# Kernel optimization log

Hardware: AMD Instinct MI355X
Metric: run time of the kernel (lower is better)

## Reference

```python
import jax, jax.numpy as jnp
import numpy as np

C = 128          # feature channels
N = 1_048_576    # octree nodes at depth 6 (divisible by 8)
M = 262_144      # full parent node count at depth 5 (incl. empty nodes)


def setup_inputs() -> dict:
    key = jax.random.key(0)
    k1, k2, k3 = jax.random.split(key, 3)
    data = jax.random.normal(k1, (C, N), dtype=jnp.float32)
    idx = jax.random.randint(k2, (M,), 0, N // 8, dtype=jnp.int32)
    empty = jax.random.uniform(k3, (M,)) < 0.5
    child_idx = jnp.where(empty, jnp.int32(-1), idx)  # -1 => empty (zero pad)
    return {"data": data, "child_idx": child_idx}


def reference(data, child_idx):
    # octree_max_pool: every 8 consecutive sibling nodes -> 1 parent value
    c, n = data.shape
    grouped = data.reshape(c, n // 8, 8)          # [C, N/8, 8]
    pooled = grouped.max(axis=-1)                  # [C, N/8]
    # octree_pad: scatter pooled non-empty parents into full parent node list,
    # zero-filling empty nodes (child_idx == -1).
    safe = jnp.clip(child_idx, 0, None)            # safe gather index
    out = jnp.where(child_idx[None, :] >= 0, pooled[:, safe], jnp.float32(0))
    return out                                     # [C, M]
```

## Files before the change

kernel.cpp:

```cpp
#include <hip/hip_runtime.h>


#define CH 128
#define CH_PER_BLOCK 8

__global__ __launch_bounds__(256) void octree_maxpool_kernel(
    const float* __restrict__ data,
    const int* __restrict__ child_idx,
    float* __restrict__ out,
    int n,
    int m_total)
{
    int m = blockIdx.x * 256 + threadIdx.x;
    if (m >= m_total) return;

    int idx = child_idx[m];
    int c0 = blockIdx.y * CH_PER_BLOCK;

    if (idx < 0) {
        #pragma unroll
        for (int cc = 0; cc < CH_PER_BLOCK; ++cc) {
            out[(size_t)(c0 + cc) * m_total + m] = 0.0f;
        }
        return;
    }

    size_t base = (size_t)idx * 8;
    #pragma unroll
    for (int cc = 0; cc < CH_PER_BLOCK; ++cc) {
        const float4* p = (const float4*)(data + (size_t)(c0 + cc) * n + base);
        float4 a = p[0];
        float4 b = p[1];
        float v = fmaxf(fmaxf(fmaxf(a.x, a.y), fmaxf(a.z, a.w)),
                        fmaxf(fmaxf(b.x, b.y), fmaxf(b.z, b.w)));
        out[(size_t)(c0 + cc) * m_total + m] = v;
    }
}

extern "C" void kernel_launch(void* const* d_in, const int* in_sizes, int n_in,
                              void* d_out, int out_size, void* d_ws, size_t ws_size,
                              hipStream_t stream) {
    const float* data      = (const float*)d_in[0];
    const int*   child_idx = (const int*)d_in[1];
    float*       out       = (float*)d_out;

    int n = in_sizes[0] / CH;
    int m = in_sizes[1];

    dim3 block(256, 1, 1);
    dim3 grid((m + 255) / 256, CH / CH_PER_BLOCK, 1);
    hipLaunchKernelGGL(octree_maxpool_kernel, grid, block, 0, stream,
                       data, child_idx, out, n, m);
}
```

Measured before the change: 864.8 us.

## Split into streaming pool pass and small gather-pad pass via workspace

The fused kernel is replaced by two kernels whenever the workspace is large enough. The first streams the whole input contiguously and writes an 8x smaller pooled buffer. The second gathers single floats from that pooled buffer, which is compact enough to stay largely in cache, and zero-fills the empty parents. This swaps random 32-byte gathers from the large input for one coalesced pass plus gathers from a small buffer, at the cost of reading data that empty nodes never use and an extra kernel launch. The fused path remains as a fallback when the workspace is too small.

New measurement: 833.6 us. 3.6% less time.

```diff
diff --git a/kernel.cpp b/kernel.cpp
--- a/kernel.cpp
+++ b/kernel.cpp
@@ -4,36 +4,69 @@
 #define CH 128
 #define CH_PER_BLOCK 8
 
-__global__ __launch_bounds__(256) void octree_maxpool_kernel(
+__global__ __launch_bounds__(256) void pool_kernel(
     const float* __restrict__ data,
+    float* __restrict__ pooled,
+    int total_groups)
+{
+    int g = blockIdx.x * 256 + threadIdx.x;
+    if (g >= total_groups) return;
+    const float4* p = (const float4*)(data + (size_t)g * 8);
+    float4 a = p[0];
+    float4 b = p[1];
+    pooled[g] = fmaxf(fmaxf(fmaxf(a.x, a.y), fmaxf(a.z, a.w)),
+                      fmaxf(fmaxf(b.x, b.y), fmaxf(b.z, b.w)));
+}
+
+__global__ __launch_bounds__(256) void pad_kernel(
+    const float* __restrict__ pooled,
     const int* __restrict__ child_idx,
     float* __restrict__ out,
-    int n,
+    int groups_per_ch,
     int m_total)
 {
     int m = blockIdx.x * 256 + threadIdx.x;
     if (m >= m_total) return;
-
     int idx = child_idx[m];
     int c0 = blockIdx.y * CH_PER_BLOCK;
 
     if (idx < 0) {
         #pragma unroll
-        for (int cc = 0; cc < CH_PER_BLOCK; ++cc) {
+        for (int cc = 0; cc < CH_PER_BLOCK; ++cc)
             out[(size_t)(c0 + cc) * m_total + m] = 0.0f;
-        }
+    } else {
+        #pragma unroll
+        for (int cc = 0; cc < CH_PER_BLOCK; ++cc)
+            out[(size_t)(c0 + cc) * m_total + m] =
+                pooled[(size_t)(c0 + cc) * groups_per_ch + idx];
+    }
+}
+
+__global__ __launch_bounds__(256) void fused_kernel(
+    const float* __restrict__ data,
+    const int* __restrict__ child_idx,
+    float* __restrict__ out,
+    int n, int m_total)
+{
+    int m = blockIdx.x * 256 + threadIdx.x;
+    if (m >= m_total) return;
+    int idx = child_idx[m];
+    int c0 = blockIdx.y * CH_PER_BLOCK;
+    if (idx < 0) {
+        #pragma unroll
+        for (int cc = 0; cc < CH_PER_BLOCK; ++cc)
+            out[(size_t)(c0 + cc) * m_total + m] = 0.0f;
         return;
     }
-
     size_t base = (size_t)idx * 8;
     #pragma unroll
     for (int cc = 0; cc < CH_PER_BLOCK; ++cc) {
         const float4* p = (const float4*)(data + (size_t)(c0 + cc) * n + base);
         float4 a = p[0];
         float4 b = p[1];
-        float v = fmaxf(fmaxf(fmaxf(a.x, a.y), fmaxf(a.z, a.w)),
-                        fmaxf(fmaxf(b.x, b.y), fmaxf(b.z, b.w)));
-        out[(size_t)(c0 + cc) * m_total + m] = v;
+        out[(size_t)(c0 + cc) * m_total + m] =
+            fmaxf(fmaxf(fmaxf(a.x, a.y), fmaxf(a.z, a.w)),
+                  fmaxf(fmaxf(b.x, b.y), fmaxf(b.z, b.w)));
     }
 }
 
@@ -46,9 +79,18 @@
 
     int n = in_sizes[0] / CH;
     int m = in_sizes[1];
+    int gpc = n / 8;
+    int total_groups = CH * gpc;
+    size_t pooled_bytes = (size_t)total_groups * sizeof(float);
 
-    dim3 block(256, 1, 1);
-    dim3 grid((m + 255) / 256, CH / CH_PER_BLOCK, 1);
-    hipLaunchKernelGGL(octree_maxpool_kernel, grid, block, 0, stream,
-                       data, child_idx, out, n, m);
+    if (ws_size >= pooled_bytes) {
+        float* pooled = (float*)d_ws;
+        dim3 b1(256), g1((total_groups + 255) / 256);
+        hipLaunchKernelGGL(pool_kernel, g1, b1, 0, stream, data, pooled, total_groups);
+        dim3 b2(256), g2((m + 255) / 256, CH / CH_PER_BLOCK);
+        hipLaunchKernelGGL(pad_kernel, g2, b2, 0, stream, pooled, child_idx, out, gpc, m);
+    } else {
+        dim3 b(256), g((m + 255) / 256, CH / CH_PER_BLOCK);
+        hipLaunchKernelGGL(fused_kernel, g, b, 0, stream, data, child_idx, out, n, m);
+    }
 }
```
